# Performance work log

Measured on AMD Instinct MI355X. Metric: run time of the kernel, lower is better.

The kernel has to match this reference:

```python
import jax, jax.numpy as jnp
import numpy as np

N = 100_000      # nodes
E = 1_600_000    # edges (avg degree 16)
D = 64           # input_dim == hidden_dim
C = 10           # output classes
G = 512          # graphs in batch
L = 5            # num_layers (L-1 = 4 GINConv layers)
BN_EPS = 1e-5


def setup_inputs() -> dict:
    key = jax.random.key(0)
    ks = jax.random.split(key, 16)
    x = jax.random.normal(ks[0], (N, D), dtype=jnp.float32)
    edge_index = jax.random.randint(ks[1], (2, E), 0, N, dtype=jnp.int32)
    batch = jnp.sort(jax.random.randint(ks[2], (N,), 0, G, dtype=jnp.int32))
    s = 1.0 / np.sqrt(D)
    Lc = L - 1
    return {
        "x": x,
        "edge_index": edge_index,
        "batch": batch,
        "eps": jnp.zeros((Lc,), jnp.float32),                                   # GINConv eps (train_eps, init 0)
        "W1": jax.random.uniform(ks[3], (Lc, D, D), jnp.float32, -s, s),        # MLP linear 1
        "b1": jax.random.uniform(ks[4], (Lc, D), jnp.float32, -s, s),
        "g1": jnp.ones((Lc, D), jnp.float32),                                   # MLP BatchNorm
        "be1": jnp.zeros((Lc, D), jnp.float32),
        "W2": jax.random.uniform(ks[5], (Lc, D, D), jnp.float32, -s, s),        # MLP linear 2
        "b2": jax.random.uniform(ks[6], (Lc, D), jnp.float32, -s, s),
        "gout": jnp.ones((Lc, D), jnp.float32),                                 # outer BatchNorm
        "beout": jnp.zeros((Lc, D), jnp.float32),
        "Wp": jax.random.uniform(ks[7], (L, D, C), jnp.float32, -s, s),         # prediction linears
        "bp": jax.random.uniform(ks[8], (L, C), jnp.float32, -s, s),
    }


def _batchnorm(h, gamma, beta):
    # training-mode BN over node dim, biased variance (torch semantics)
    m = jnp.mean(h, axis=0)
    v = jnp.mean(jnp.square(h - m), axis=0)
    return gamma * (h - m) * jax.lax.rsqrt(v + BN_EPS) + beta


def reference(x, edge_index, batch, eps, W1, b1, g1, be1, W2, b2, gout, beout, Wp, bp):
    src, dst = edge_index[0], edge_index[1]
    hidden_rep = [x]
    h = x
    for l in range(L - 1):
        # GINConv: (1 + eps) * x + scatter-add of neighbor features
        agg = jax.ops.segment_sum(h[src], dst, num_segments=N)
        z = (1.0 + eps[l]) * h + agg
        # 2-layer MLP with internal BN+ReLU
        z = z @ W1[l] + b1[l]
        z = jax.nn.relu(_batchnorm(z, g1[l], be1[l]))
        z = z @ W2[l] + b2[l]
        # outer BN + ReLU
        h = jax.nn.relu(_batchnorm(z, gout[l], beout[l]))
        hidden_rep.append(h)
    # jumping-knowledge readout: per-layer global_add_pool + linear (dropout off / eval)
    score = jnp.zeros((G, C), jnp.float32)
    for l, hl in enumerate(hidden_rep):
        pooled = jax.ops.segment_sum(hl, batch, num_segments=G)
        score = score + pooled @ Wp[l] + bp[l]
    return score
```

## Files before the change

kernel.cpp:

```cpp
#include <hip/hip_runtime.h>

#define NN 100000
#define EE 1600000
#define DD 64
#define CC 10
#define GG 512
#define LL 5
#define NPAD 100352
#define N64 (NN * DD)
#define NB 392
#define PCH 4096
#define BCAP 6144
#define SC 8

typedef short bf16x8 __attribute__((ext_vector_type(8)));
typedef float f32x4  __attribute__((ext_vector_type(4)));
union U16 { uint4 u; bf16x8 h; };

__device__ __forceinline__ float bits2f(unsigned int b) { return __uint_as_float(b); }
__device__ __forceinline__ float bf2f(unsigned short s) { return __uint_as_float((unsigned int)s << 16); }
__device__ __forceinline__ unsigned short f2bf_rne(float v) {
    unsigned int b = __float_as_uint(v);
    return (unsigned short)((b + 0x7fffu + ((b >> 16) & 1u)) >> 16);
}
__device__ __forceinline__ void unpack8(uint4 u, float* f) {
    f[0] = bits2f(u.x << 16); f[1] = bits2f(u.x & 0xffff0000u);
    f[2] = bits2f(u.y << 16); f[3] = bits2f(u.y & 0xffff0000u);
    f[4] = bits2f(u.z << 16); f[5] = bits2f(u.z & 0xffff0000u);
    f[6] = bits2f(u.w << 16); f[7] = bits2f(u.w & 0xffff0000u);
}
__device__ __forceinline__ uint4 pack8(const float* f) {
    uint4 u;
    u.x = (unsigned int)f2bf_rne(f[0]) | ((unsigned int)f2bf_rne(f[1]) << 16);
    u.y = (unsigned int)f2bf_rne(f[2]) | ((unsigned int)f2bf_rne(f[3]) << 16);
    u.z = (unsigned int)f2bf_rne(f[4]) | ((unsigned int)f2bf_rne(f[5]) << 16);
    u.w = (unsigned int)f2bf_rne(f[6]) | ((unsigned int)f2bf_rne(f[7]) << 16);
    return u;
}
__device__ __forceinline__ void acc8(uint4 u, float* a) {
    float t[8];
    unpack8(u, t);
    #pragma unroll
    for (int k = 0; k < 8; ++k) a[k] += t[k];
}

__global__ __launch_bounds__(256) void prep_x_pool_k(
    const float* __restrict__ x, const int* __restrict__ batch,
    unsigned short* __restrict__ hb, float* __restrict__ pooled)
{
    int t = threadIdx.x;
    int f = t & 63;
    int q = t >> 6;
    int n0 = blockIdx.x * 64 + q * 16;
    int nmax = NN - n0; if (nmax > 16) nmax = 16;
    float acc = 0.f;
    int curg = -1;
    #pragma unroll 4
    for (int i = 0; i < nmax; ++i) {
        int n = n0 + i;
        int g = batch[n];
        if (g != curg) {
            if (curg >= 0) atomicAdd(&pooled[(size_t)curg * DD + f], acc);
            acc = 0.f; curg = g;
        }
        float v = x[(size_t)n * DD + f];
        hb[(size_t)n * DD + f] = f2bf_rne(v);
        acc += v;
    }
    if (curg >= 0) atomicAdd(&pooled[(size_t)curg * DD + f], acc);
}

__global__ __launch_bounds__(256) void prep_w_k(const float* __restrict__ W1,
                                                const float* __restrict__ W2,
                                                unsigned short* __restrict__ wt) {
    int mat = blockIdx.x;
    const float* src = (mat < 4) ? (W1 + (size_t)mat * 4096)
                                 : (W2 + (size_t)(mat - 4) * 4096);
    for (int idx = threadIdx.x; idx < 4096; idx += 256) {
        int c = idx >> 6, k = idx & 63;
        wt[(size_t)mat * 4096 + c * 64 + k] = f2bf_rne(src[k * 64 + c]);
    }
}

__global__ __launch_bounds__(256) void bhist_k(const int* __restrict__ ei,
                                               int* __restrict__ bh) {
    __shared__ int cnt[NB];
    for (int i = threadIdx.x; i < NB; i += 256) cnt[i] = 0;
    __syncthreads();
    int stride = gridDim.x * 256;
    for (int e = blockIdx.x * 256 + threadIdx.x; e < EE; e += stride)
        atomicAdd(&cnt[ei[EE + e] >> 8], 1);
    __syncthreads();
    for (int i = threadIdx.x; i < NB; i += 256)
        if (cnt[i]) atomicAdd(&bh[i], cnt[i]);
}

__global__ __launch_bounds__(512) void bscan_k(const int* __restrict__ bh,
                                               int* __restrict__ bo,
                                               int* __restrict__ bcur) {
    __shared__ int s[512];
    int t = threadIdx.x;
    int v = (t < NB) ? bh[t] : 0;
    s[t] = v;
    __syncthreads();
    for (int d = 1; d < 512; d <<= 1) {
        int a = (t >= d) ? s[t - d] : 0;
        __syncthreads();
        s[t] += a;
        __syncthreads();
    }
    int excl = s[t] - v;
    if (t < NB) { bo[t] = excl; bcur[t] = excl; }
    if (t == NB - 1) bo[NB] = excl + v;
}

__global__ __launch_bounds__(256) void partition_k(const int* __restrict__ ei,
                                                   int* __restrict__ bcur,
                                                   unsigned int* __restrict__ stage) {
    __shared__ int hist[NB];
    __shared__ int base[NB];
    __shared__ int gbase[NB];
    __shared__ int cnt2[NB];
    __shared__ int scanbuf[512];
    __shared__ unsigned int pairs[PCH];
    __shared__ unsigned short pbkt[PCH];
    int t = threadIdx.x;
    int e0 = blockIdx.x * PCH;
    int nE = EE - e0; if (nE > PCH) nE = PCH;

    for (int i = t; i < NB; i += 256) { hist[i] = 0; cnt2[i] = 0; }
    __syncthreads();

    int mys[16], myd[16];
    #pragma unroll
    for (int i = 0; i < 16; ++i) {
        int idx = i * 256 + t;
        if (idx < nE) {
            mys[i] = ei[e0 + idx];
            myd[i] = ei[EE + e0 + idx];
            atomicAdd(&hist[myd[i] >> 8], 1);
        } else myd[i] = -1;
    }
    __syncthreads();

    scanbuf[t]       = (t < NB) ? hist[t] : 0;
    scanbuf[t + 256] = (t + 256 < NB) ? hist[t + 256] : 0;
    __syncthreads();
    for (int d = 1; d < 512; d <<= 1) {
        int a0 = (t >= d) ? scanbuf[t - d] : 0;
        int a1 = ((t + 256) >= d) ? scanbuf[t + 256 - d] : 0;
        __syncthreads();
        scanbuf[t] += a0;
        scanbuf[t + 256] += a1;
        __syncthreads();
    }
    if (t < NB)       base[t]       = scanbuf[t] - hist[t];
    if (t + 256 < NB) base[t + 256] = scanbuf[t + 256] - hist[t + 256];
    __syncthreads();

    #pragma unroll
    for (int i = 0; i < 16; ++i) {
        if (myd[i] >= 0) {
            int b = myd[i] >> 8;
            int p = base[b] + atomicAdd(&cnt2[b], 1);
            pairs[p] = (unsigned)mys[i] | ((unsigned)(myd[i] & 255) << 17);
            pbkt[p] = (unsigned short)b;
        }
    }
    __syncthreads();
    for (int i = t; i < NB; i += 256)
        if (hist[i]) gbase[i] = atomicAdd(&bcur[i], hist[i]);
    __syncthreads();
    for (int p = t; p < nE; p += 256) {
        int b = pbkt[p];
        stage[gbase[b] + (p - base[b])] = pairs[p];
    }
}

__global__ __launch_bounds__(256) void bucket_csr_k(const unsigned int* __restrict__ stage,
                                                    const int* __restrict__ bo,
                                                    int* __restrict__ adj,
                                                    int* __restrict__ offs) {
    __shared__ int deg[256];
    __shared__ int sb[256];
    __shared__ int nb_[256];
    __shared__ int c2[256];
    __shared__ int loc[BCAP];
    int b = blockIdx.x;
    int s0 = bo[b], s1 = bo[b + 1];
    int cnt = s1 - s0;
    int t = threadIdx.x;

    deg[t] = 0;
    __syncthreads();
    for (int i = t; i < cnt; i += 256) atomicAdd(&deg[(stage[s0 + i] >> 17) & 255], 1);
    __syncthreads();
    sb[t] = deg[t];
    __syncthreads();
    for (int d = 1; d < 256; d <<= 1) {
        int a = (t >= d) ? sb[t - d] : 0;
        __syncthreads();
        sb[t] += a;
        __syncthreads();
    }
    int nbase = sb[t] - deg[t];
    nb_[t] = nbase;
    c2[t] = 0;
    offs[b * 256 + t] = s0 + nbase;
    __syncthreads();

    if (cnt <= BCAP) {
        for (int i = t; i < cnt; i += 256) {
            unsigned int pr = stage[s0 + i];
            int ln = (pr >> 17) & 255;
            int p = nb_[ln] + atomicAdd(&c2[ln], 1);
            loc[p] = (int)(pr & 0x1FFFF);
        }
        __syncthreads();
        for (int i = t; i < cnt; i += 256) adj[s0 + i] = loc[i];
    } else {
        for (int i = t; i < cnt; i += 256) {
            unsigned int pr = stage[s0 + i];
            int ln = (pr >> 17) & 255;
            int p = nb_[ln] + atomicAdd(&c2[ln], 1);
            adj[s0 + p] = (int)(pr & 0x1FFFF);
        }
    }
}

__global__ __launch_bounds__(512, 8) void layer1_k(
    const unsigned short* __restrict__ hb, const int* __restrict__ adj,
    const int* __restrict__ offs, const float* __restrict__ epsArr, int l,
    const unsigned short* __restrict__ wtm, const float* __restrict__ bias,
    unsigned short* __restrict__ z1, float* __restrict__ stats1,
    float* __restrict__ stats2z)
{
    __shared__ unsigned short aLDS[64 * 64];
    const int t = threadIdx.x;
    const int lane = t & 63;
    const int w = t >> 6;
    const int n15 = lane & 15;
    const int quad = lane >> 4;

    if (blockIdx.x < SC && t < 128) stats2z[blockIdx.x * 128 + t] = 0.f;

    const float epsv = 1.0f + epsArr[l];
    const int c8 = lane & 7;
    {
        int lr = w * 8 + (lane >> 3);
        int n = blockIdx.x * 64 + lr;
        float acc[8] = {0.f,0.f,0.f,0.f,0.f,0.f,0.f,0.f};
        if (n < NN) {
            uint4 a = *(const uint4*)(hb + (size_t)n * DD + c8 * 8);
            unpack8(a, acc);
            #pragma unroll
            for (int j2 = 0; j2 < 8; ++j2) acc[j2] *= epsv;
            int j = offs[n], end = offs[n + 1];
            #pragma unroll 1
            for (; j + 3 < end; j += 4) {
                int s0 = adj[j], s1 = adj[j + 1], s2 = adj[j + 2], s3 = adj[j + 3];
                uint4 v0 = *(const uint4*)(hb + (size_t)s0 * DD + c8 * 8);
                uint4 v1 = *(const uint4*)(hb + (size_t)s1 * DD + c8 * 8);
                uint4 v2 = *(const uint4*)(hb + (size_t)s2 * DD + c8 * 8);
                uint4 v3 = *(const uint4*)(hb + (size_t)s3 * DD + c8 * 8);
                acc8(v0, acc); acc8(v1, acc); acc8(v2, acc); acc8(v3, acc);
            }
            #pragma unroll 1
            for (; j < end; ++j) {
                uint4 v0 = *(const uint4*)(hb + (size_t)adj[j] * DD + c8 * 8);
                acc8(v0, acc);
            }
        }
        int pu = c8 ^ (lr & 7);
        *(uint4*)(aLDS + lr * 64 + pu * 8) = pack8(acc);
    }

    const int rt = w & 3;
    const int cb = (w >> 2) * 2;
    U16 bfr[2][2];
    #pragma unroll
    for (int ci = 0; ci < 2; ++ci)
        #pragma unroll
        for (int ks = 0; ks < 2; ++ks)
            bfr[ci][ks].u = *(const uint4*)(wtm + (size_t)((cb + ci) * 16 + n15) * 64 + ks * 32 + quad * 8);

    __syncthreads();

    U16 afr[2];
    int lr2 = rt * 16 + n15;
    #pragma unroll
    for (int ks = 0; ks < 2; ++ks) {
        int pu = (ks * 4 + quad) ^ (lr2 & 7);
        afr[ks].u = *(const uint4*)(aLDS + lr2 * 64 + pu * 8);
    }

    const int rowg0 = blockIdx.x * 64 + rt * 16;
    const int copy = blockIdx.x & (SC - 1);
    #pragma unroll
    for (int ci = 0; ci < 2; ++ci) {
        int ct = cb + ci;
        f32x4 acc = {0.f, 0.f, 0.f, 0.f};
        acc = __builtin_amdgcn_mfma_f32_16x16x32_bf16(afr[0].h, bfr[ci][0].h, acc, 0, 0, 0);
        acc = __builtin_amdgcn_mfma_f32_16x16x32_bf16(afr[1].h, bfr[ci][1].h, acc, 0, 0, 0);
        int col = ct * 16 + n15;
        float bcol = bias[col];
        float s = 0.f, ss = 0.f;
        #pragma unroll
        for (int r = 0; r < 4; ++r) {
            int rg = rowg0 + quad * 4 + r;
            float v = acc[r] + bcol;
            if (rg < NN) {
                z1[(size_t)rg * DD + col] = f2bf_rne(v);
                s += v;
                ss = fmaf(v, v, ss);
            }
        }
        s  += __shfl_xor(s, 16, 64);  s  += __shfl_xor(s, 32, 64);
        ss += __shfl_xor(ss, 16, 64); ss += __shfl_xor(ss, 32, 64);
        if (lane < 16) {
            atomicAdd(&stats1[copy * 128 + ct * 16 + lane], s);
            atomicAdd(&stats1[copy * 128 + 64 + ct * 16 + lane], ss);
        }
    }
}

__global__ __launch_bounds__(256) void layer2_k(
    const unsigned short* __restrict__ z1, const float* __restrict__ stats1,
    const float* __restrict__ gamma, const float* __restrict__ beta, int off,
    const unsigned short* __restrict__ wtm, const float* __restrict__ bias,
    unsigned short* __restrict__ z2, float* __restrict__ stats2)
{
    __shared__ float ssS[128];
    const int t = threadIdx.x;
    const int lane = t & 63;
    const int w = t >> 6;
    const int n15 = lane & 15;
    const int quad = lane >> 4;
    const int rowg0 = blockIdx.x * 64 + w * 16;

    U16 bfr[4][2];
    #pragma unroll
    for (int ct = 0; ct < 4; ++ct)
        #pragma unroll
        for (int ks = 0; ks < 2; ++ks)
            bfr[ct][ks].u = *(const uint4*)(wtm + (size_t)(ct * 16 + n15) * 64 + ks * 32 + quad * 8);

    int arow = rowg0 + n15;
    int arowc = (arow < NN) ? arow : (NN - 1);
    uint4 raw[2];
    #pragma unroll
    for (int ks = 0; ks < 2; ++ks)
        raw[ks] = *(const uint4*)(z1 + (size_t)arowc * DD + ks * 32 + quad * 8);

    if (t < 64) {
        float S = 0.f, SS = 0.f;
        #pragma unroll
        for (int c = 0; c < SC; ++c) { S += stats1[c * 128 + t]; SS += stats1[c * 128 + 64 + t]; }
        float inv_n = 1.0f / (float)NN;
        float mean = S * inv_n;
        float var  = SS * inv_n - mean * mean;
        float sc = gamma[off + t] * rsqrtf(var + 1e-5f);
        ssS[t] = sc;
        ssS[64 + t] = beta[off + t] - sc * mean;
    }
    __syncthreads();

    U16 afr[2];
    #pragma unroll
    for (int ks = 0; ks < 2; ++ks) {
        float f[8];
        unpack8(raw[ks], f);
        int k0 = ks * 32 + quad * 8;
        #pragma unroll
        for (int j = 0; j < 8; ++j)
            f[j] = fmaxf(fmaf(ssS[k0 + j], f[j], ssS[64 + k0 + j]), 0.f);
        afr[ks].u = pack8(f);
    }

    const int copy = blockIdx.x & (SC - 1);
    #pragma unroll
    for (int ct = 0; ct < 4; ++ct) {
        f32x4 acc = {0.f, 0.f, 0.f, 0.f};
        acc = __builtin_amdgcn_mfma_f32_16x16x32_bf16(afr[0].h, bfr[ct][0].h, acc, 0, 0, 0);
        acc = __builtin_amdgcn_mfma_f32_16x16x32_bf16(afr[1].h, bfr[ct][1].h, acc, 0, 0, 0);
        int col = ct * 16 + n15;
        float bcol = bias[col];
        float s = 0.f, ss = 0.f;
        #pragma unroll
        for (int r = 0; r < 4; ++r) {
            int rg = rowg0 + quad * 4 + r;
            float v = acc[r] + bcol;
            if (rg < NN) {
                z2[(size_t)rg * DD + col] = f2bf_rne(v);
                s += v;
                ss = fmaf(v, v, ss);
            }
        }
        s  += __shfl_xor(s, 16, 64);  s  += __shfl_xor(s, 32, 64);
        ss += __shfl_xor(ss, 16, 64); ss += __shfl_xor(ss, 32, 64);
        if (lane < 16) {
            atomicAdd(&stats2[copy * 128 + ct * 16 + lane], s);
            atomicAdd(&stats2[copy * 128 + 64 + ct * 16 + lane], ss);
        }
    }
}

__global__ __launch_bounds__(256) void layer3_k(
    const unsigned short* __restrict__ z2, const float* __restrict__ stats2,
    const float* __restrict__ gamma, const float* __restrict__ beta, int off,
    const int* __restrict__ batch, unsigned short* __restrict__ hout,
    float* __restrict__ pooled, float* __restrict__ stats1z)
{
    __shared__ float ssS[128];
    int t = threadIdx.x;
    if (blockIdx.x < SC && t < 128) stats1z[blockIdx.x * 128 + t] = 0.f;
    if (t < 64) {
        float S = 0.f, SS = 0.f;
        #pragma unroll
        for (int c = 0; c < SC; ++c) { S += stats2[c * 128 + t]; SS += stats2[c * 128 + 64 + t]; }
        float inv_n = 1.0f / (float)NN;
        float mean = S * inv_n;
        float var  = SS * inv_n - mean * mean;
        float sc = gamma[off + t] * rsqrtf(var + 1e-5f);
        ssS[t] = sc;
        ssS[64 + t] = beta[off + t] - sc * mean;
    }
    __syncthreads();

    int f = t & 63;
    int q = t >> 6;
    int n0 = blockIdx.x * 64 + q * 16;
    int nmax = NN - n0; if (nmax > 16) nmax = 16;
    float sc = ssS[f], sh = ssS[64 + f];
    float acc = 0.f;
    int curg = -1;
    #pragma unroll 4
    for (int i = 0; i < nmax; ++i) {
        int n = n0 + i;
        int g = batch[n];
        if (g != curg) {
            if (curg >= 0) atomicAdd(&pooled[(size_t)curg * DD + f], acc);
            acc = 0.f; curg = g;
        }
        float v = bf2f(z2[(size_t)n * DD + f]);
        v = fmaxf(fmaf(sc, v, sh), 0.f);
        hout[(size_t)n * DD + f] = f2bf_rne(v);
        acc += v;
    }
    if (curg >= 0) atomicAdd(&pooled[(size_t)curg * DD + f], acc);
}

__global__ void readout_k(const float* __restrict__ pooled,
                          const float* __restrict__ Wp, const float* __restrict__ bp,
                          float* __restrict__ out)
{
    int gc = blockIdx.x * blockDim.x + threadIdx.x;
    if (gc >= GG * CC) return;
    int g = gc / CC, c = gc - g * CC;
    float acc = 0.f;
    for (int l = 0; l < LL; ++l) {
        acc += bp[l * CC + c];
        const float* p  = pooled + ((size_t)l * GG + g) * DD;
        const float* wv = Wp + (size_t)l * DD * CC + c;
        #pragma unroll 8
        for (int f = 0; f < DD; ++f) acc = fmaf(p[f], wv[f * CC], acc);
    }
    out[gc] = acc;
}

extern "C" void kernel_launch(void* const* d_in, const int* in_sizes, int n_in,
                              void* d_out, int out_size, void* d_ws, size_t ws_size,
                              hipStream_t stream) {
    const float* x     = (const float*)d_in[0];
    const int*   ei    = (const int*)d_in[1];
    const int*   batch = (const int*)d_in[2];
    const float* eps   = (const float*)d_in[3];
    const float* W1    = (const float*)d_in[4];
    const float* b1    = (const float*)d_in[5];
    const float* g1    = (const float*)d_in[6];
    const float* be1   = (const float*)d_in[7];
    const float* W2    = (const float*)d_in[8];
    const float* b2    = (const float*)d_in[9];
    const float* gout  = (const float*)d_in[10];
    const float* beout = (const float*)d_in[11];
    const float* Wp    = (const float*)d_in[12];
    const float* bp    = (const float*)d_in[13];
    float* out = (float*)d_out;

    unsigned int* stage = (unsigned int*)d_ws;
    int* adj   = (int*)(stage + EE);
    int* offs  = adj + EE;
    int* bh    = offs + NPAD + 256;
    int* bo    = bh + 400;
    int* bcur  = bo + 400;
    float* pooled = (float*)(bcur + 400);
    float* stats1 = pooled + (size_t)LL * GG * DD;
    float* stats2 = stats1 + SC * 128;
    unsigned short* hb  = (unsigned short*)(stats2 + SC * 128);
    unsigned short* z1b = hb + N64;
    unsigned short* z2b = z1b + N64;
    unsigned short* wt  = z2b + N64;

    hipMemsetAsync(pooled, 0, ((size_t)LL * GG * DD + 2 * SC * 128) * sizeof(float), stream);
    prep_x_pool_k<<<(NN + 63) / 64, 256, 0, stream>>>(x, batch, hb, pooled);
    prep_w_k<<<8, 256, 0, stream>>>(W1, W2, wt);

    hipMemsetAsync(bh, 0, NB * sizeof(int), stream);
    bhist_k<<<512, 256, 0, stream>>>(ei, bh);
    bscan_k<<<1, 512, 0, stream>>>(bh, bo, bcur);
    partition_k<<<(EE + PCH - 1) / PCH, 256, 0, stream>>>(ei, bcur, stage);
    bucket_csr_k<<<NB, 256, 0, stream>>>(stage, bo, adj, offs);

    const int gemm_grid = (NN + 63) / 64;
    const int node_grid = (NN + 63) / 64;
    for (int l = 0; l < LL - 1; ++l) {
        layer1_k<<<gemm_grid, 512, 0, stream>>>(
            hb, adj, offs, eps, l, wt + (size_t)l * 4096, b1 + l * DD, z1b, stats1, stats2);
        layer2_k<<<gemm_grid, 256, 0, stream>>>(
            z1b, stats1, g1, be1, l * DD, wt + (size_t)(4 + l) * 4096, b2 + l * DD, z2b, stats2);
        layer3_k<<<node_grid, 256, 0, stream>>>(
            z2b, stats2, gout, beout, l * DD, batch, hb,
            pooled + (size_t)(l + 1) * GG * DD, stats1);
    }
    readout_k<<<(GG * CC + 255) / 256, 256, 0, stream>>>(pooled, Wp, bp, out);
}
```

Measured before the change: 620.7 us.

## Merge prep kernels and memsets into one launch; software-pipeline neighbor index loads

Result: faster. 581.7 us (-6.3%).

```diff
diff --git a/kernel.cpp b/kernel.cpp
--- a/kernel.cpp
+++ b/kernel.cpp
@@ -12,6 +12,7 @@
 #define PCH 4096
 #define BCAP 6144
 #define SC 8
+#define PREPG 1563
 
 typedef short bf16x8 __attribute__((ext_vector_type(8)));
 typedef float f32x4  __attribute__((ext_vector_type(4)));
@@ -44,55 +45,54 @@
     for (int k = 0; k < 8; ++k) a[k] += t[k];
 }
 
-__global__ __launch_bounds__(256) void prep_x_pool_k(
+__global__ __launch_bounds__(256) void prep_all_k(
     const float* __restrict__ x, const int* __restrict__ batch,
-    unsigned short* __restrict__ hb, float* __restrict__ pooled)
+    unsigned short* __restrict__ hbuf, float* __restrict__ pooled,
+    const float* __restrict__ W1, const float* __restrict__ W2,
+    unsigned short* __restrict__ wt,
+    const int* __restrict__ ei, int* __restrict__ bh)
 {
-    int t = threadIdx.x;
-    int f = t & 63;
-    int q = t >> 6;
-    int n0 = blockIdx.x * 64 + q * 16;
-    int nmax = NN - n0; if (nmax > 16) nmax = 16;
-    float acc = 0.f;
-    int curg = -1;
-    #pragma unroll 4
-    for (int i = 0; i < nmax; ++i) {
-        int n = n0 + i;
-        int g = batch[n];
-        if (g != curg) {
-            if (curg >= 0) atomicAdd(&pooled[(size_t)curg * DD + f], acc);
-            acc = 0.f; curg = g;
-        }
-        float v = x[(size_t)n * DD + f];
-        hb[(size_t)n * DD + f] = f2bf_rne(v);
-        acc += v;
-    }
-    if (curg >= 0) atomicAdd(&pooled[(size_t)curg * DD + f], acc);
-}
-
-__global__ __launch_bounds__(256) void prep_w_k(const float* __restrict__ W1,
-                                                const float* __restrict__ W2,
-                                                unsigned short* __restrict__ wt) {
-    int mat = blockIdx.x;
-    const float* src = (mat < 4) ? (W1 + (size_t)mat * 4096)
-                                 : (W2 + (size_t)(mat - 4) * 4096);
-    for (int idx = threadIdx.x; idx < 4096; idx += 256) {
-        int c = idx >> 6, k = idx & 63;
-        wt[(size_t)mat * 4096 + c * 64 + k] = f2bf_rne(src[k * 64 + c]);
-    }
-}
-
-__global__ __launch_bounds__(256) void bhist_k(const int* __restrict__ ei,
-                                               int* __restrict__ bh) {
     __shared__ int cnt[NB];
-    for (int i = threadIdx.x; i < NB; i += 256) cnt[i] = 0;
-    __syncthreads();
-    int stride = gridDim.x * 256;
-    for (int e = blockIdx.x * 256 + threadIdx.x; e < EE; e += stride)
-        atomicAdd(&cnt[ei[EE + e] >> 8], 1);
-    __syncthreads();
-    for (int i = threadIdx.x; i < NB; i += 256)
-        if (cnt[i]) atomicAdd(&bh[i], cnt[i]);
+    const int bid = blockIdx.x;
+    const int t = threadIdx.x;
+    if (bid < PREPG) {
+        int f = t & 63;
+        int q = t >> 6;
+        int n0 = bid * 64 + q * 16;
+        int nmax = NN - n0; if (nmax > 16) nmax = 16;
+        float acc = 0.f;
+        int curg = -1;
+        #pragma unroll 4
+        for (int i = 0; i < nmax; ++i) {
+            int n = n0 + i;
+            int g = batch[n];
+            if (g != curg) {
+                if (curg >= 0) atomicAdd(&pooled[(size_t)curg * DD + f], acc);
+                acc = 0.f; curg = g;
+            }
+            float v = x[(size_t)n * DD + f];
+            hbuf[(size_t)n * DD + f] = f2bf_rne(v);
+            acc += v;
+        }
+        if (curg >= 0) atomicAdd(&pooled[(size_t)curg * DD + f], acc);
+    } else if (bid < PREPG + 8) {
+        int mat = bid - PREPG;
+        const float* src = (mat < 4) ? (W1 + (size_t)mat * 4096)
+                                     : (W2 + (size_t)(mat - 4) * 4096);
+        for (int idx = t; idx < 4096; idx += 256) {
+            int c = idx >> 6, k = idx & 63;
+            wt[(size_t)mat * 4096 + c * 64 + k] = f2bf_rne(src[k * 64 + c]);
+        }
+    } else {
+        int hid = bid - PREPG - 8;
+        for (int i = t; i < NB; i += 256) cnt[i] = 0;
+        __syncthreads();
+        for (int e = hid * 256 + t; e < EE; e += 512 * 256)
+            atomicAdd(&cnt[ei[EE + e] >> 8], 1);
+        __syncthreads();
+        for (int i = t; i < NB; i += 256)
+            if (cnt[i]) atomicAdd(&bh[i], cnt[i]);
+    }
 }
 
 __global__ __launch_bounds__(512) void bscan_k(const int* __restrict__ bh,
@@ -256,19 +256,31 @@
             #pragma unroll
             for (int j2 = 0; j2 < 8; ++j2) acc[j2] *= epsv;
             int j = offs[n], end = offs[n + 1];
-            #pragma unroll 1
-            for (; j + 3 < end; j += 4) {
-                int s0 = adj[j], s1 = adj[j + 1], s2 = adj[j + 2], s3 = adj[j + 3];
-                uint4 v0 = *(const uint4*)(hb + (size_t)s0 * DD + c8 * 8);
-                uint4 v1 = *(const uint4*)(hb + (size_t)s1 * DD + c8 * 8);
-                uint4 v2 = *(const uint4*)(hb + (size_t)s2 * DD + c8 * 8);
-                uint4 v3 = *(const uint4*)(hb + (size_t)s3 * DD + c8 * 8);
-                acc8(v0, acc); acc8(v1, acc); acc8(v2, acc); acc8(v3, acc);
-            }
-            #pragma unroll 1
-            for (; j < end; ++j) {
-                uint4 v0 = *(const uint4*)(hb + (size_t)adj[j] * DD + c8 * 8);
-                acc8(v0, acc);
+            if (j < end) {
+                int e1 = end - 1;
+                int a0 = adj[j];
+                int a1 = adj[(j + 1 < end) ? j + 1 : e1];
+                int a2 = adj[(j + 2 < end) ? j + 2 : e1];
+                int a3 = adj[(j + 3 < end) ? j + 3 : e1];
+                #pragma unroll 1
+                while (j < end) {
+                    uint4 v0 = *(const uint4*)(hb + (size_t)a0 * DD + c8 * 8);
+                    uint4 v1 = *(const uint4*)(hb + (size_t)a1 * DD + c8 * 8);
+                    uint4 v2 = *(const uint4*)(hb + (size_t)a2 * DD + c8 * 8);
+                    uint4 v3 = *(const uint4*)(hb + (size_t)a3 * DD + c8 * 8);
+                    int jn = j + 4;
+                    int b0 = adj[(jn     < end) ? jn     : e1];
+                    int b1 = adj[(jn + 1 < end) ? jn + 1 : e1];
+                    int b2 = adj[(jn + 2 < end) ? jn + 2 : e1];
+                    int b3 = adj[(jn + 3 < end) ? jn + 3 : e1];
+                    int rem = end - j;
+                    acc8(v0, acc);
+                    if (rem > 1) acc8(v1, acc);
+                    if (rem > 2) acc8(v2, acc);
+                    if (rem > 3) acc8(v3, acc);
+                    a0 = b0; a1 = b1; a2 = b2; a3 = b3;
+                    j = jn;
+                }
             }
         }
         int pu = c8 ^ (lr & 7);
@@ -490,10 +502,10 @@
     unsigned int* stage = (unsigned int*)d_ws;
     int* adj   = (int*)(stage + EE);
     int* offs  = adj + EE;
-    int* bh    = offs + NPAD + 256;
-    int* bo    = bh + 400;
+    int* bo    = offs + NPAD + 256;
     int* bcur  = bo + 400;
-    float* pooled = (float*)(bcur + 400);
+    int* bh    = bcur + 400;
+    float* pooled = (float*)(bh + 400);
     float* stats1 = pooled + (size_t)LL * GG * DD;
     float* stats2 = stats1 + SC * 128;
     unsigned short* hb  = (unsigned short*)(stats2 + SC * 128);
@@ -501,12 +513,8 @@
     unsigned short* z2b = z1b + N64;
     unsigned short* wt  = z2b + N64;
 
-    hipMemsetAsync(pooled, 0, ((size_t)LL * GG * DD + 2 * SC * 128) * sizeof(float), stream);
-    prep_x_pool_k<<<(NN + 63) / 64, 256, 0, stream>>>(x, batch, hb, pooled);
-    prep_w_k<<<8, 256, 0, stream>>>(W1, W2, wt);
-
-    hipMemsetAsync(bh, 0, NB * sizeof(int), stream);
-    bhist_k<<<512, 256, 0, stream>>>(ei, bh);
+    hipMemsetAsync(bh, 0, (400 + (size_t)LL * GG * DD + 2 * SC * 128) * sizeof(int), stream);
+    prep_all_k<<<PREPG + 8 + 512, 256, 0, stream>>>(x, batch, hb, pooled, W1, W2, wt, ei, bh);
     bscan_k<<<1, 512, 0, stream>>>(bh, bo, bcur);
     partition_k<<<(EE + PCH - 1) / PCH, 256, 0, stream>>>(ei, bcur, stage);
     bucket_csr_k<<<NB, 256, 0, stream>>>(stage, bo, adj, offs);
```
